# Kernel optimization log

Hardware: AMD Instinct MI355X
Metric: run time of the kernel (lower is better)

## Reference

```python
import jax, jax.numpy as jnp
import numpy as np

N = 2000  # nodes per graph (hardcoded in the original module)


def gatv2(x, src, dst, edge_attr, Wl, Wr, We, att, b):
    """PyG GATv2Conv (concat=True, negative_slope=0.2, edge_dim) forward.
    x: [N, Fin]; src/dst: [E]; edge_attr: [E, 2]; att: [H, C]. Returns [N, H*C]."""
    n = x.shape[0]
    H, C = att.shape
    xl = (x @ Wl).reshape(n, H, C)            # messages from source nodes
    xr = (x @ Wr).reshape(n, H, C)            # target-node term
    ee = (edge_attr @ We).reshape(-1, H, C)   # edge feature term
    m = jax.nn.leaky_relu(xl[src] + xr[dst] + ee, 0.2)
    logits = jnp.einsum('ehc,hc->eh', m, att)           # [E, H]
    lmax = jax.ops.segment_max(logits, dst, num_segments=n)
    p = jnp.exp(logits - lmax[dst])
    denom = jax.ops.segment_sum(p, dst, num_segments=n)
    alpha = p / (denom[dst] + 1e-16)                    # scatter-softmax over in-edges
    out = jax.ops.segment_sum(alpha[:, :, None] * xl[src], dst, num_segments=n)
    return out.reshape(n, H * C) + b


def setup_inputs() -> dict:
    key = jax.random.key(0)
    ks = jax.random.split(key, 32)
    B, T, F, E = 4, 10, 8, 16000
    s = 0.05
    d = {
        'x': jax.random.normal(ks[0], (B, T, N, F), jnp.float32),
        'edge_index': jax.random.randint(ks[1], (2, E), 0, N, jnp.int32),
        'edge_attr': jax.random.normal(ks[2], (E, 2), jnp.float32),
        'w_l0': s * jax.random.normal(ks[3], (8, 128)),
        'w_r0': s * jax.random.normal(ks[4], (8, 128)),
        'w_e0': s * jax.random.normal(ks[5], (2, 128)),
        'att0': s * jax.random.normal(ks[6], (4, 32)),
        'b0': s * jax.random.normal(ks[7], (128,)),
        'w_l1': s * jax.random.normal(ks[8], (128, 128)),
        'w_r1': s * jax.random.normal(ks[9], (128, 128)),
        'w_e1': s * jax.random.normal(ks[10], (2, 128)),
        'att1': s * jax.random.normal(ks[11], (4, 32)),
        'b1': s * jax.random.normal(ks[12], (128,)),
        'w_l2': s * jax.random.normal(ks[13], (128, 32)),
        'w_r2': s * jax.random.normal(ks[14], (128, 32)),
        'w_e2': s * jax.random.normal(ks[15], (2, 32)),
        'att2': s * jax.random.normal(ks[16], (4, 8)),
        'b2': s * jax.random.normal(ks[17], (32,)),
        'w_ih': s * jax.random.normal(ks[18], (1024, 64000)),
        'w_hh': s * jax.random.normal(ks[19], (1024, 256)),
        'b_ih': s * jax.random.normal(ks[20], (1024,)),
        'b_hh': s * jax.random.normal(ks[21], (1024,)),
        'fc1_w': s * jax.random.normal(ks[22], (256, 512)),
        'fc1_b': s * jax.random.normal(ks[23], (512,)),
        'fc2_w': s * jax.random.normal(ks[24], (512, 1)),
        'fc2_b': s * jax.random.normal(ks[25], (1,)),
    }
    return d


def reference(x, edge_index, edge_attr, w_l0, w_r0, w_e0, att0, b0,
              w_l1, w_r1, w_e1, att1, b1, w_l2, w_r2, w_e2, att2, b2,
              w_ih, w_hh, b_ih, b_hh, fc1_w, fc1_b, fc2_w, fc2_b):
    B, T = x.shape[0], x.shape[1]
    # PyG GATv2Conv add_self_loops=True with fill_value='mean' for edge_attr
    loop = jnp.arange(N, dtype=edge_index.dtype)
    src = jnp.concatenate([edge_index[0], loop])
    dst = jnp.concatenate([edge_index[1], loop])
    ea = jnp.concatenate([edge_attr, jnp.broadcast_to(edge_attr.mean(0), (N, 2))], axis=0)

    def gat_stack(xt):  # [N, F] -> [N*32] flattened embedding
        h = jax.nn.relu(gatv2(xt, src, dst, ea, w_l0, w_r0, w_e0, att0, b0))
        h = jax.nn.relu(gatv2(h, src, dst, ea, w_l1, w_r1, w_e1, att1, b1))
        h = jax.nn.relu(gatv2(h, src, dst, ea, w_l2, w_r2, w_e2, att2, b2))
        return h.reshape(-1)

    emb = jax.vmap(jax.vmap(gat_stack))(x)  # [B, T, 64000]

    # single-layer LSTM (torch gate order: i, f, g, o)
    Hh = w_hh.shape[1]
    def step(carry, xt):
        h, c = carry
        g = xt @ w_ih.T + h @ w_hh.T + (b_ih + b_hh)
        i, f, gg, o = jnp.split(g, 4, axis=-1)
        c = jax.nn.sigmoid(f) * c + jax.nn.sigmoid(i) * jnp.tanh(gg)
        h = jax.nn.sigmoid(o) * jnp.tanh(c)
        return (h, c), h
    h0 = jnp.zeros((B, Hh), emb.dtype)
    (_, _), hs = jax.lax.scan(step, (h0, h0), jnp.swapaxes(emb, 0, 1))  # hs: [T, B, Hh]

    last = jax.nn.relu(hs[-1])                       # relu(lstm_out)[:, -1, :]
    hid = jax.nn.relu(last @ fc1_w + fc1_b)          # (dropout=0 -> identity)
    return hid @ fc2_w + fc2_b                       # [B, 1]
```

## Files before the change

### kernel.cpp

```cpp
#include <hip/hip_runtime.h>
#include <hip/hip_bf16.h>
#include <math.h>

typedef __hip_bfloat16 bf16;
typedef __attribute__((ext_vector_type(8))) short short8;
typedef __attribute__((ext_vector_type(4))) float f32x4;

#define NNODES 2000
#define NEDGE_IN 16000
#define NEDGE 18000
#define NGRAPH 40

__device__ __forceinline__ float bf2f(bf16 v){ return __bfloat162float(v); }
__device__ __forceinline__ bf16 f2bf(float v){ return __float2bfloat16(v); }
__device__ __forceinline__ short bfbits(float v){ bf16 t = __float2bfloat16(v); return *reinterpret_cast<short*>(&t); }
__device__ __forceinline__ float blo(unsigned u){ return __uint_as_float(u<<16); }
__device__ __forceinline__ float bhi(unsigned u){ return __uint_as_float(u & 0xffff0000u); }

__global__ __launch_bounds__(256) void k_setup(const float* __restrict__ ea, float* __restrict__ mean_ea,
                        const float* __restrict__ whh, unsigned* __restrict__ whhT2,
                        const float* __restrict__ w1a, const float* __restrict__ w1b,
                        const float* __restrict__ w2a, const float* __restrict__ w2b,
                        bf16* __restrict__ b1a, bf16* __restrict__ b1b,
                        bf16* __restrict__ b2a, bf16* __restrict__ b2b,
                        int* __restrict__ cnt, int* __restrict__ cursor, float* __restrict__ gates){
  int bb = blockIdx.x, tid = threadIdx.x;
  if (bb == 0){
    __shared__ float s0l[256], s1l[256];
    float s0=0.f, s1=0.f;
    for (int e = tid; e < NEDGE_IN; e += 256){ s0 += ea[2*e]; s1 += ea[2*e+1]; }
    s0l[tid]=s0; s1l[tid]=s1; __syncthreads();
    for (int d=128; d>=1; d>>=1){
      if (tid < d){ s0l[tid]+=s0l[tid+d]; s1l[tid]+=s1l[tid+d]; }
      __syncthreads();
    }
    if (tid==0){ mean_ea[0]=s0l[0]/(float)NEDGE_IN; mean_ea[1]=s1l[0]/(float)NEDGE_IN; }
  } else if (bb < 513){
    int idx = (bb-1)*256 + tid;
    int j = idx >> 7, kp = idx & 127;
    unsigned ulo = (unsigned)(unsigned short)bfbits(whh[j*256 + 2*kp]);
    unsigned uhi = (unsigned)(unsigned short)bfbits(whh[j*256 + 2*kp + 1]);
    whhT2[kp*1024 + j] = (uhi<<16) | ulo;
  } else if (bb < 673){
    int idx = (bb-513)*256 + tid;
    const float* src; bf16* dst; int n, local;
    if (idx < 16384){ src=w1a; dst=b1a; n=128; local=idx; }
    else if (idx < 32768){ src=w1b; dst=b1b; n=128; local=idx-16384; }
    else if (idx < 36864){ src=w2a; dst=b2a; n=32; local=idx-32768; }
    else { src=w2b; dst=b2b; n=32; local=idx-36864; }
    int k = local / n, c = local % n;
    dst[c*128 + k] = f2bf(src[local]);
  } else {
    int idx = (bb-673)*256 + tid;
    if (idx < 2000) cnt[idx] = 0;
    else if (idx < 4000) cursor[idx-2000] = 0;
    else if (idx < 44960) gates[idx-4000] = 0.f;
  }
}

__global__ void k_count(const int* __restrict__ ei, int* __restrict__ cnt){
  int e = blockIdx.x*256 + threadIdx.x;
  if (e >= NEDGE) return;
  int d = (e < NEDGE_IN) ? ei[NEDGE_IN + e] : (e - NEDGE_IN);
  atomicAdd(&cnt[d], 1);
}

__global__ void k_scan(const int* __restrict__ cnt, int* __restrict__ off){
  __shared__ int s[2048];
  int lane = threadIdx.x;
  for (int i = lane; i < 2048; i += 64) s[i] = (i < NNODES) ? cnt[i] : 0;
  __syncthreads();
  int base = lane*32, run = 0;
  for (int j=0;j<32;j++){ int t = s[base+j]; s[base+j] = run; run += t; }
  int x = run;
  for (int d=1; d<64; d<<=1){ int y = __shfl_up(x, d); if (lane >= d) x += y; }
  int chunkOff = x - run;
  for (int j=0;j<32;j++){ int idx = base+j; if (idx <= NNODES) off[idx] = chunkOff + s[idx]; }
}

__global__ void k_scatter(const int* __restrict__ ei, const int* __restrict__ off,
                          int* __restrict__ cursor, const float* __restrict__ ea,
                          const float* __restrict__ mean_ea,
                          int* __restrict__ csr_src, float2* __restrict__ eaP){
  int e = blockIdx.x*256 + threadIdx.x;
  if (e >= NEDGE) return;
  int d, sn; float2 a;
  if (e < NEDGE_IN){ sn = ei[e]; d = ei[NEDGE_IN+e]; a = ((const float2*)ea)[e]; }
  else { sn = e-NEDGE_IN; d = sn; a.x = mean_ea[0]; a.y = mean_ea[1]; }
  int p = off[d] + atomicAdd(&cursor[d], 1);
  csr_src[p] = sn;
  eaP[p] = a;
}

__global__ __launch_bounds__(256) void k_gemm0(const float* __restrict__ X, const float* __restrict__ Wa,
                                               const float* __restrict__ Wb,
                                               bf16* __restrict__ Ya, bf16* __restrict__ Yb){
  __shared__ float Ws[2*8*128];
  for (int i = threadIdx.x; i < 8*128; i += 256){ Ws[i] = Wa[i]; Ws[1024+i] = Wb[i]; }
  __syncthreads();
  int j  = threadIdx.x % 128;
  int rg = threadIdx.x / 128;
  size_t m0 = (size_t)blockIdx.x*8 + (size_t)rg*4;
  const float* x0 = X + m0*8;
  float a0=0.f,a1=0.f,a2=0.f,a3=0.f, b0=0.f,b1=0.f,b2=0.f,b3=0.f;
  #pragma unroll
  for (int k=0;k<8;k++){
    float wa = Ws[k*128 + j], wb = Ws[1024 + k*128 + j];
    float x_0 = x0[k], x_1 = x0[8+k], x_2 = x0[16+k], x_3 = x0[24+k];
    a0 += x_0*wa; a1 += x_1*wa; a2 += x_2*wa; a3 += x_3*wa;
    b0 += x_0*wb; b1 += x_1*wb; b2 += x_2*wb; b3 += x_3*wb;
  }
  bf16* ya = Ya + m0*128 + j;
  bf16* yb = Yb + m0*128 + j;
  ya[0]=f2bf(a0); ya[128]=f2bf(a1); ya[256]=f2bf(a2); ya[384]=f2bf(a3);
  yb[0]=f2bf(b0); yb[128]=f2bf(b1); yb[256]=f2bf(b2); yb[384]=f2bf(b3);
}

template<int N>
__global__ __launch_bounds__(256) void k_gemm_mf2(const bf16* __restrict__ A, const bf16* __restrict__ BTa,
                                                  const bf16* __restrict__ BTb,
                                                  bf16* __restrict__ Ya, bf16* __restrict__ Yb){
  const int NT = N/16;
  int lane = threadIdx.x & 63, wv = threadIdx.x >> 6;
  size_t m0 = (size_t)blockIdx.x*128 + (size_t)wv*32;
  int r = lane & 15, kg = lane >> 4;
  const f32x4 zero = {0.f,0.f,0.f,0.f};
  f32x4 acca[2][NT], accb[2][NT];
  #pragma unroll
  for (int s=0;s<2;s++)
    #pragma unroll
    for (int t=0;t<NT;t++){ acca[s][t] = zero; accb[s][t] = zero; }
  #pragma unroll
  for (int c=0;c<4;c++){
    short8 a0 = *(const short8*)(A + (m0 + r)*128 + c*32 + kg*8);
    short8 a1 = *(const short8*)(A + (m0 + 16 + r)*128 + c*32 + kg*8);
    #pragma unroll
    for (int t=0;t<NT;t++){
      short8 ba = *(const short8*)(BTa + (size_t)(t*16 + r)*128 + c*32 + kg*8);
      short8 bb = *(const short8*)(BTb + (size_t)(t*16 + r)*128 + c*32 + kg*8);
      acca[0][t] = __builtin_amdgcn_mfma_f32_16x16x32_bf16(a0, ba, acca[0][t], 0,0,0);
      acca[1][t] = __builtin_amdgcn_mfma_f32_16x16x32_bf16(a1, ba, acca[1][t], 0,0,0);
      accb[0][t] = __builtin_amdgcn_mfma_f32_16x16x32_bf16(a0, bb, accb[0][t], 0,0,0);
      accb[1][t] = __builtin_amdgcn_mfma_f32_16x16x32_bf16(a1, bb, accb[1][t], 0,0,0);
    }
  }
  #pragma unroll
  for (int s=0;s<2;s++)
    #pragma unroll
    for (int t=0;t<NT;t++){
      size_t row = m0 + s*16 + kg*4;
      int col = t*16 + r;
      #pragma unroll
      for (int i=0;i<4;i++){
        Ya[(row+i)*N + col] = f2bf(acca[s][t][i]);
        Yb[(row+i)*N + col] = f2bf(accb[s][t][i]);
      }
    }
}

__global__ __launch_bounds__(256) void k_edge_g(const bf16* __restrict__ XL, const bf16* __restrict__ XR,
                                                const float2* __restrict__ eaP, const int* __restrict__ off,
                                                const int* __restrict__ csr_src, const float* __restrict__ att,
                                                const float* __restrict__ We, const float* __restrict__ bias,
                                                bf16* __restrict__ Hout){
  int tid = threadIdx.x;
  int ln = tid & 63;
  int gq = tid >> 6;
  int n  = blockIdx.x;
  int c0 = 2*ln;
  float av0 = att[c0], av1 = att[c0+1];
  float w00 = We[c0], w01 = We[c0+1];
  float w10 = We[128+c0], w11 = We[128+c0+1];
  const unsigned* XLu = (const unsigned*)XL;
  const unsigned* XRu = (const unsigned*)XR;
  float xr0[10], xr1[10], srun[10], acc0[10], acc1[10];
  #pragma unroll
  for (int t=0;t<10;t++){
    int g = gq*10 + t;
    unsigned xu = XRu[((size_t)g*NNODES + n)*64 + ln];
    xr0[t] = blo(xu); xr1[t] = bhi(xu);
    srun[t]=0.f; acc0[t]=0.f; acc1[t]=0.f;
  }
  int p0 = off[n], p1 = off[n+1];
  for (int p = p0; p < p1; ++p){
    int u = csr_src[p];
    float2 e = eaP[p];
    float ed0 = fmaf(e.x, w00, e.y*w10);
    float ed1 = fmaf(e.x, w01, e.y*w11);
    unsigned xl[10];
    #pragma unroll
    for (int t=0;t<10;t++){
      int g = gq*10 + t;
      xl[t] = XLu[((size_t)g*NNODES + u)*64 + ln];
    }
    #pragma unroll
    for (int t=0;t<10;t++){
      float x0 = blo(xl[t]), x1 = bhi(xl[t]);
      float s0 = x0 + xr0[t] + ed0;
      float s1 = x1 + xr1[t] + ed1;
      float m0 = s0>0.f?s0:0.2f*s0, m1 = s1>0.f?s1:0.2f*s1;
      float c = fmaf(m0, av0, m1*av1);
      #pragma unroll
      for (int d=8; d>=1; d>>=1) c += __shfl_xor(c, d);
      float pe = __expf(c);
      srun[t] += pe;
      acc0[t] = fmaf(pe, x0, acc0[t]);
      acc1[t] = fmaf(pe, x1, acc1[t]);
    }
  }
  #pragma unroll
  for (int t=0;t<10;t++){
    int g = gq*10 + t;
    float inv = 1.f/(srun[t] + 1e-16f);
    float o0 = fmaf(acc0[t], inv, bias[c0]);
    float o1 = fmaf(acc1[t], inv, bias[c0+1]);
    o0 = o0>0.f?o0:0.f; o1 = o1>0.f?o1:0.f;
    unsigned r0 = (unsigned)(unsigned short)bfbits(o0);
    unsigned r1 = (unsigned)(unsigned short)bfbits(o1);
    ((unsigned*)Hout)[((size_t)g*NNODES + n)*64 + ln] = (r1<<16) | r0;
  }
}

template<int H, int C>
__global__ __launch_bounds__(256) void k_edge(const bf16* __restrict__ XL, const bf16* __restrict__ XR,
                                              const float2* __restrict__ eaP, const int* __restrict__ off,
                                              const int* __restrict__ csr_src, const float* __restrict__ att,
                                              const float* __restrict__ We, const float* __restrict__ bias,
                                              bf16* __restrict__ Hout){
  const int HC = H*C;
  const int LPN = HC/2;
  const int NPW = 64/LPN;
  const int NPB = 4*NPW;
  int tid = threadIdx.x;
  int lane = tid & 63, wv = tid >> 6;
  int ln = lane % LPN;
  int n  = blockIdx.x*NPB + wv*NPW + lane/LPN;
  int g  = blockIdx.y;
  int c0 = 2*ln;
  size_t gbase = (size_t)g*NNODES*HC;
  const unsigned* XLu = (const unsigned*)(XL + gbase);
  unsigned xru = ((const unsigned*)(XR + gbase))[n*LPN + ln];
  float xr0 = blo(xru), xr1 = bhi(xru);
  float av0 = att[c0], av1 = att[c0+1];
  float w00 = We[c0], w01 = We[c0+1];
  float w10 = We[HC+c0], w11 = We[HC+c0+1];
  float srun = 0.f, acc0 = 0.f, acc1 = 0.f;
  int p0 = off[n], p1 = off[n+1];
  int p = p0;
  for (; p+2 <= p1; p += 2){
    int uA = csr_src[p], uB = csr_src[p+1];
    float2 eA = eaP[p], eB = eaP[p+1];
    unsigned xlA = XLu[uA*LPN + ln];
    unsigned xlB = XLu[uB*LPN + ln];
    float xa0 = blo(xlA), xa1 = bhi(xlA);
    float xb0 = blo(xlB), xb1 = bhi(xlB);
    float sa0 = xa0 + fmaf(eA.x,w00, fmaf(eA.y,w10, xr0));
    float sa1 = xa1 + fmaf(eA.x,w01, fmaf(eA.y,w11, xr1));
    float sb0 = xb0 + fmaf(eB.x,w00, fmaf(eB.y,w10, xr0));
    float sb1 = xb1 + fmaf(eB.x,w01, fmaf(eB.y,w11, xr1));
    float ma0 = sa0>0.f?sa0:0.2f*sa0, ma1 = sa1>0.f?sa1:0.2f*sa1;
    float mb0 = sb0>0.f?sb0:0.2f*sb0, mb1 = sb1>0.f?sb1:0.2f*sb1;
    float cA = fmaf(ma0,av0, ma1*av1);
    float cB = fmaf(mb0,av0, mb1*av1);
    #pragma unroll
    for (int d=C/4; d>=1; d>>=1){ cA += __shfl_xor(cA, d); cB += __shfl_xor(cB, d); }
    float peA = __expf(cA), peB = __expf(cB);
    srun += peA + peB;
    acc0 = fmaf(peA, xa0, fmaf(peB, xb0, acc0));
    acc1 = fmaf(peA, xa1, fmaf(peB, xb1, acc1));
  }
  if (p < p1){
    int uA = csr_src[p];
    float2 eA = eaP[p];
    unsigned xlA = XLu[uA*LPN + ln];
    float xa0 = blo(xlA), xa1 = bhi(xlA);
    float sa0 = xa0 + fmaf(eA.x,w00, fmaf(eA.y,w10, xr0));
    float sa1 = xa1 + fmaf(eA.x,w01, fmaf(eA.y,w11, xr1));
    float ma0 = sa0>0.f?sa0:0.2f*sa0, ma1 = sa1>0.f?sa1:0.2f*sa1;
    float cA = fmaf(ma0,av0, ma1*av1);
    #pragma unroll
    for (int d=C/4; d>=1; d>>=1) cA += __shfl_xor(cA, d);
    float peA = __expf(cA);
    srun += peA;
    acc0 = fmaf(peA, xa0, acc0);
    acc1 = fmaf(peA, xa1, acc1);
  }
  float inv = 1.f/(srun + 1e-16f);
  float o0 = fmaf(acc0, inv, bias[c0]);
  float o1 = fmaf(acc1, inv, bias[c0+1]);
  o0 = o0>0.f?o0:0.f; o1 = o1>0.f?o1:0.f;
  unsigned r0 = (unsigned)(unsigned short)bfbits(o0);
  unsigned r1 = (unsigned)(unsigned short)bfbits(o1);
  ((unsigned*)(Hout + gbase))[n*LPN + ln] = (r1<<16) | r0;
}

#define GATES_KS 40
__global__ __launch_bounds__(256) void k_gates_mf(const bf16* __restrict__ emb, const float* __restrict__ wih,
                                                  float* __restrict__ gates){
  const int nk = 2000/GATES_KS;
  int lane = threadIdx.x & 63, wv = threadIdx.x >> 6;
  int r = lane & 15, kg = lane >> 4;
  int j0 = (blockIdx.x*4 + wv)*16;
  int k0 = blockIdx.y*nk*32;
  const f32x4 zero = {0.f,0.f,0.f,0.f};
  f32x4 acc0 = zero, acc1 = zero, acc2 = zero;
  const float* wrow = wih + (size_t)(j0 + r)*64000;
  const bf16*  e0p  = emb + (size_t)r*64000;
  const bf16*  e1p  = emb + (size_t)(16+r)*64000;
  const bf16*  e2p  = emb + (size_t)(32+r)*64000;
  #pragma unroll 2
  for (int s=0; s<nk; ++s){
    int k = k0 + s*32 + kg*8;
    float4 wa = *(const float4*)(wrow + k);
    float4 wb = *(const float4*)(wrow + k + 4);
    short8 bfr;
    bfr[0]=bfbits(wa.x); bfr[1]=bfbits(wa.y); bfr[2]=bfbits(wa.z); bfr[3]=bfbits(wa.w);
    bfr[4]=bfbits(wb.x); bfr[5]=bfbits(wb.y); bfr[6]=bfbits(wb.z); bfr[7]=bfbits(wb.w);
    short8 a0 = *(const short8*)(e0p + k);
    short8 a1 = *(const short8*)(e1p + k);
    short8 a2 = *(const short8*)(e2p + k);
    acc0 = __builtin_amdgcn_mfma_f32_16x16x32_bf16(a0, bfr, acc0, 0,0,0);
    acc1 = __builtin_amdgcn_mfma_f32_16x16x32_bf16(a1, bfr, acc1, 0,0,0);
    acc2 = __builtin_amdgcn_mfma_f32_16x16x32_bf16(a2, bfr, acc2, 0,0,0);
  }
  int col = j0 + r;
  #pragma unroll
  for (int i=0;i<4;i++){
    int row = kg*4 + i;
    atomicAdd(&gates[(size_t)row*1024 + col], acc0[i]);
    atomicAdd(&gates[(size_t)(row+16)*1024 + col], acc1[i]);
    if (row + 32 < 40) atomicAdd(&gates[(size_t)(row+32)*1024 + col], acc2[i]);
  }
}

__global__ __launch_bounds__(1024) void k_lstm10(const float* __restrict__ gates, const unsigned* __restrict__ whhT2,
                                                 const float* __restrict__ bih, const float* __restrict__ bhh,
                                                 float* __restrict__ hst){
  __shared__ float hs[256];
  __shared__ float g[1024];
  int b = blockIdx.x, j = threadIdx.x;
  float c_reg = 0.f;
  if (j < 256) hs[j] = 0.f;
  float bias = bih[j] + bhh[j];
  __syncthreads();
  for (int t=0;t<10;t++){
    float acc = gates[(size_t)(b*10+t)*1024 + j] + bias;
    #pragma unroll 16
    for (int kp=0;kp<128;kp++){
      unsigned u = whhT2[kp*1024 + j];
      float2 h2 = *(const float2*)&hs[2*kp];
      acc = fmaf(blo(u), h2.x, acc);
      acc = fmaf(bhi(u), h2.y, acc);
    }
    g[j] = acc;
    __syncthreads();
    if (j < 256){
      float i_ = g[j], f_ = g[j+256], gg = g[j+512], o_ = g[j+768];
      float si = 1.f/(1.f+__expf(-i_));
      float sf = 1.f/(1.f+__expf(-f_));
      float so = 1.f/(1.f+__expf(-o_));
      c_reg = sf*c_reg + si*tanhf(gg);
      float hn = so*tanhf(c_reg);
      hs[j] = hn;
      if (t==9) hst[b*256+j] = hn;
    }
    __syncthreads();
  }
}

__global__ __launch_bounds__(512) void k_head(const float* __restrict__ hst, const float* __restrict__ fc1w,
                                              const float* __restrict__ fc1b, const float* __restrict__ fc2w,
                                              const float* __restrict__ fc2b, float* __restrict__ out){
  __shared__ float r[512];
  int b = blockIdx.x, j = threadIdx.x;
  float acc = fc1b[j];
  for (int k=0;k<256;k++){
    float l = hst[b*256+k]; l = l>0.f?l:0.f;
    acc += l * fc1w[k*512 + j];
  }
  float hid = acc>0.f?acc:0.f;
  r[j] = hid * fc2w[j];
  __syncthreads();
  for (int d=256; d>=1; d>>=1){ if (j<d) r[j]+=r[j+d]; __syncthreads(); }
  if (j==0) out[b] = r[0] + fc2b[0];
}

extern "C" void kernel_launch(void* const* d_in, const int* in_sizes, int n_in,
                              void* d_out, int out_size, void* d_ws, size_t ws_size,
                              hipStream_t stream){
  const float* x    = (const float*)d_in[0];
  const int*   ei   = (const int*)  d_in[1];
  const float* ea   = (const float*)d_in[2];
  const float* wl0  = (const float*)d_in[3];
  const float* wr0  = (const float*)d_in[4];
  const float* we0  = (const float*)d_in[5];
  const float* att0 = (const float*)d_in[6];
  const float* b0   = (const float*)d_in[7];
  const float* wl1  = (const float*)d_in[8];
  const float* wr1  = (const float*)d_in[9];
  const float* we1  = (const float*)d_in[10];
  const float* att1 = (const float*)d_in[11];
  const float* b1   = (const float*)d_in[12];
  const float* wl2  = (const float*)d_in[13];
  const float* wr2  = (const float*)d_in[14];
  const float* we2  = (const float*)d_in[15];
  const float* att2 = (const float*)d_in[16];
  const float* b2   = (const float*)d_in[17];
  const float* wih  = (const float*)d_in[18];
  const float* whh  = (const float*)d_in[19];
  const float* bih  = (const float*)d_in[20];
  const float* bhh  = (const float*)d_in[21];
  const float* fc1w = (const float*)d_in[22];
  const float* fc1b = (const float*)d_in[23];
  const float* fc2w = (const float*)d_in[24];
  const float* fc2b = (const float*)d_in[25];
  float* out = (float*)d_out;

  char* base = (char*)d_ws; size_t cur = 0;
  auto alloc = [&](size_t bytes)->void*{
    cur = (cur + 255) & ~(size_t)255; void* p = base + cur; cur += bytes; return p;
  };
  float* mean_ea = (float*)alloc(8);
  int*   cnt     = (int*)  alloc((size_t)NNODES*4);
  int*   off     = (int*)  alloc((size_t)(NNODES+1)*4);
  int*   cursor  = (int*)  alloc((size_t)NNODES*4);
  int*   csr_src = (int*)  alloc((size_t)NEDGE*4);
  float2* eaP    = (float2*)alloc((size_t)NEDGE*8);
  bf16*  XL      = (bf16*) alloc((size_t)80000*128*2);
  bf16*  XR      = (bf16*) alloc((size_t)80000*128*2);
  bf16*  HBUF    = (bf16*) alloc((size_t)80000*128*2);
  float* gates   = (float*)alloc((size_t)40*1024*4);
  float* hst     = (float*)alloc(4*256*4);
  unsigned* whhT2= (unsigned*)alloc((size_t)128*1024*4);
  bf16*  bt1a    = (bf16*) alloc((size_t)128*128*2);
  bf16*  bt1b    = (bf16*) alloc((size_t)128*128*2);
  bf16*  bt2a    = (bf16*) alloc((size_t)32*128*2);
  bf16*  bt2b    = (bf16*) alloc((size_t)32*128*2);

  k_setup <<<849,256,0,stream>>>(ea, mean_ea, whh, whhT2, wl1, wr1, wl2, wr2,
                                 bt1a, bt1b, bt2a, bt2b, cnt, cursor, gates);
  k_count   <<<(NEDGE+255)/256,256,0,stream>>>(ei, cnt);
  k_scan    <<<1,64,0,stream>>>(cnt, off);
  k_scatter <<<(NEDGE+255)/256,256,0,stream>>>(ei, off, cursor, ea, mean_ea, csr_src, eaP);

  k_gemm0   <<<10000,256,0,stream>>>(x, wl0, wr0, XL, XR);
  k_edge_g  <<<NNODES,256,0,stream>>>(XL,XR,eaP,off,csr_src,att0,we0,b0,HBUF);

  k_gemm_mf2<128> <<<625,256,0,stream>>>(HBUF, bt1a, bt1b, XL, XR);
  k_edge_g  <<<NNODES,256,0,stream>>>(XL,XR,eaP,off,csr_src,att1,we1,b1,HBUF);

  k_gemm_mf2<32> <<<625,256,0,stream>>>(HBUF, bt2a, bt2b, XL, XR);
  k_edge<4,8> <<<dim3(125,40),256,0,stream>>>(XL,XR,eaP,off,csr_src,att2,we2,b2,HBUF);

  k_gates_mf<<<dim3(16,GATES_KS),256,0,stream>>>(HBUF, wih, gates);

  k_lstm10<<<4,1024,0,stream>>>(gates, whhT2, bih, bhh, hst);

  k_head<<<4,512,0,stream>>>(hst, fc1w, fc1b, fc2w, fc2b, out);
}
```

Baseline: 417.7 us.

## Fuse gemm0 into setup, split-K gates with partial buffer, fuse LSTM with head

The layer-0 projection GEMM is merged into the setup kernel as extra blocks, which removes one launch. The gates split-K count doubles and atomicAdd accumulation is replaced by per-split partial writes plus a separate reduction kernel, which also drops the gates zeroing. The LSTM and the FC head are merged into one kernel. Leaky-relu and relu selects become fmaxf. The cost is an extra reduction pass over a larger partial buffer, in exchange for more parallelism in the gates GEMM and no atomic contention.

```diff
diff --git a/kernel.cpp b/kernel.cpp
--- a/kernel.cpp
+++ b/kernel.cpp
@@ -10,6 +10,7 @@
 #define NEDGE_IN 16000
 #define NEDGE 18000
 #define NGRAPH 40
+#define GATES_KS 80
 
 __device__ __forceinline__ float bf2f(bf16 v){ return __bfloat162float(v); }
 __device__ __forceinline__ bf16 f2bf(float v){ return __float2bfloat16(v); }
@@ -23,10 +24,34 @@
                         const float* __restrict__ w2a, const float* __restrict__ w2b,
                         bf16* __restrict__ b1a, bf16* __restrict__ b1b,
                         bf16* __restrict__ b2a, bf16* __restrict__ b2b,
-                        int* __restrict__ cnt, int* __restrict__ cursor, float* __restrict__ gates){
+                        int* __restrict__ cnt, int* __restrict__ cursor,
+                        const float* __restrict__ X, const float* __restrict__ Wa,
+                        const float* __restrict__ Wb,
+                        bf16* __restrict__ Ya, bf16* __restrict__ Yb){
+  __shared__ float smem[2048];
   int bb = blockIdx.x, tid = threadIdx.x;
-  if (bb == 0){
-    __shared__ float s0l[256], s1l[256];
+  if (bb >= 689){
+    int blk = bb - 689;
+    for (int i = tid; i < 1024; i += 256){ smem[i] = Wa[i]; smem[1024+i] = Wb[i]; }
+    __syncthreads();
+    int j  = tid & 127;
+    int rg = tid >> 7;
+    size_t m0 = (size_t)blk*8 + (size_t)rg*4;
+    const float* x0 = X + m0*8;
+    float a0=0.f,a1=0.f,a2=0.f,a3=0.f, b0=0.f,b1=0.f,b2=0.f,b3=0.f;
+    #pragma unroll
+    for (int k=0;k<8;k++){
+      float wa = smem[k*128 + j], wb = smem[1024 + k*128 + j];
+      float x_0 = x0[k], x_1 = x0[8+k], x_2 = x0[16+k], x_3 = x0[24+k];
+      a0 += x_0*wa; a1 += x_1*wa; a2 += x_2*wa; a3 += x_3*wa;
+      b0 += x_0*wb; b1 += x_1*wb; b2 += x_2*wb; b3 += x_3*wb;
+    }
+    bf16* ya = Ya + m0*128 + j;
+    bf16* yb = Yb + m0*128 + j;
+    ya[0]=f2bf(a0); ya[128]=f2bf(a1); ya[256]=f2bf(a2); ya[384]=f2bf(a3);
+    yb[0]=f2bf(b0); yb[128]=f2bf(b1); yb[256]=f2bf(b2); yb[384]=f2bf(b3);
+  } else if (bb == 0){
+    float* s0l = smem; float* s1l = smem + 256;
     float s0=0.f, s1=0.f;
     for (int e = tid; e < NEDGE_IN; e += 256){ s0 += ea[2*e]; s1 += ea[2*e+1]; }
     s0l[tid]=s0; s1l[tid]=s1; __syncthreads();
@@ -54,7 +79,6 @@
     int idx = (bb-673)*256 + tid;
     if (idx < 2000) cnt[idx] = 0;
     else if (idx < 4000) cursor[idx-2000] = 0;
-    else if (idx < 44960) gates[idx-4000] = 0.f;
   }
 }
 
@@ -90,30 +114,6 @@
   int p = off[d] + atomicAdd(&cursor[d], 1);
   csr_src[p] = sn;
   eaP[p] = a;
-}
-
-__global__ __launch_bounds__(256) void k_gemm0(const float* __restrict__ X, const float* __restrict__ Wa,
-                                               const float* __restrict__ Wb,
-                                               bf16* __restrict__ Ya, bf16* __restrict__ Yb){
-  __shared__ float Ws[2*8*128];
-  for (int i = threadIdx.x; i < 8*128; i += 256){ Ws[i] = Wa[i]; Ws[1024+i] = Wb[i]; }
-  __syncthreads();
-  int j  = threadIdx.x % 128;
-  int rg = threadIdx.x / 128;
-  size_t m0 = (size_t)blockIdx.x*8 + (size_t)rg*4;
-  const float* x0 = X + m0*8;
-  float a0=0.f,a1=0.f,a2=0.f,a3=0.f, b0=0.f,b1=0.f,b2=0.f,b3=0.f;
-  #pragma unroll
-  for (int k=0;k<8;k++){
-    float wa = Ws[k*128 + j], wb = Ws[1024 + k*128 + j];
-    float x_0 = x0[k], x_1 = x0[8+k], x_2 = x0[16+k], x_3 = x0[24+k];
-    a0 += x_0*wa; a1 += x_1*wa; a2 += x_2*wa; a3 += x_3*wa;
-    b0 += x_0*wb; b1 += x_1*wb; b2 += x_2*wb; b3 += x_3*wb;
-  }
-  bf16* ya = Ya + m0*128 + j;
-  bf16* yb = Yb + m0*128 + j;
-  ya[0]=f2bf(a0); ya[128]=f2bf(a1); ya[256]=f2bf(a2); ya[384]=f2bf(a3);
-  yb[0]=f2bf(b0); yb[128]=f2bf(b1); yb[256]=f2bf(b2); yb[384]=f2bf(b3);
 }
 
 template<int N>
@@ -198,7 +198,8 @@
       float x0 = blo(xl[t]), x1 = bhi(xl[t]);
       float s0 = x0 + xr0[t] + ed0;
       float s1 = x1 + xr1[t] + ed1;
-      float m0 = s0>0.f?s0:0.2f*s0, m1 = s1>0.f?s1:0.2f*s1;
+      float m0 = fmaxf(s0, 0.2f*s0);
+      float m1 = fmaxf(s1, 0.2f*s1);
       float c = fmaf(m0, av0, m1*av1);
       #pragma unroll
       for (int d=8; d>=1; d>>=1) c += __shfl_xor(c, d);
@@ -214,7 +215,7 @@
     float inv = 1.f/(srun[t] + 1e-16f);
     float o0 = fmaf(acc0[t], inv, bias[c0]);
     float o1 = fmaf(acc1[t], inv, bias[c0+1]);
-    o0 = o0>0.f?o0:0.f; o1 = o1>0.f?o1:0.f;
+    o0 = fmaxf(o0, 0.f); o1 = fmaxf(o1, 0.f);
     unsigned r0 = (unsigned)(unsigned short)bfbits(o0);
     unsigned r1 = (unsigned)(unsigned short)bfbits(o1);
     ((unsigned*)Hout)[((size_t)g*NNODES + n)*64 + ln] = (r1<<16) | r0;
@@ -258,8 +259,8 @@
     float sa1 = xa1 + fmaf(eA.x,w01, fmaf(eA.y,w11, xr1));
     float sb0 = xb0 + fmaf(eB.x,w00, fmaf(eB.y,w10, xr0));
     float sb1 = xb1 + fmaf(eB.x,w01, fmaf(eB.y,w11, xr1));
-    float ma0 = sa0>0.f?sa0:0.2f*sa0, ma1 = sa1>0.f?sa1:0.2f*sa1;
-    float mb0 = sb0>0.f?sb0:0.2f*sb0, mb1 = sb1>0.f?sb1:0.2f*sb1;
+    float ma0 = fmaxf(sa0, 0.2f*sa0), ma1 = fmaxf(sa1, 0.2f*sa1);
+    float mb0 = fmaxf(sb0, 0.2f*sb0), mb1 = fmaxf(sb1, 0.2f*sb1);
     float cA = fmaf(ma0,av0, ma1*av1);
     float cB = fmaf(mb0,av0, mb1*av1);
     #pragma unroll
@@ -276,7 +277,7 @@
     float xa0 = blo(xlA), xa1 = bhi(xlA);
     float sa0 = xa0 + fmaf(eA.x,w00, fmaf(eA.y,w10, xr0));
     float sa1 = xa1 + fmaf(eA.x,w01, fmaf(eA.y,w11, xr1));
-    float ma0 = sa0>0.f?sa0:0.2f*sa0, ma1 = sa1>0.f?sa1:0.2f*sa1;
+    float ma0 = fmaxf(sa0, 0.2f*sa0), ma1 = fmaxf(sa1, 0.2f*sa1);
     float cA = fmaf(ma0,av0, ma1*av1);
     #pragma unroll
     for (int d=C/4; d>=1; d>>=1) cA += __shfl_xor(cA, d);
@@ -288,20 +289,20 @@
   float inv = 1.f/(srun + 1e-16f);
   float o0 = fmaf(acc0, inv, bias[c0]);
   float o1 = fmaf(acc1, inv, bias[c0+1]);
-  o0 = o0>0.f?o0:0.f; o1 = o1>0.f?o1:0.f;
+  o0 = fmaxf(o0, 0.f); o1 = fmaxf(o1, 0.f);
   unsigned r0 = (unsigned)(unsigned short)bfbits(o0);
   unsigned r1 = (unsigned)(unsigned short)bfbits(o1);
   ((unsigned*)(Hout + gbase))[n*LPN + ln] = (r1<<16) | r0;
 }
 
-#define GATES_KS 40
 __global__ __launch_bounds__(256) void k_gates_mf(const bf16* __restrict__ emb, const float* __restrict__ wih,
-                                                  float* __restrict__ gates){
+                                                  float* __restrict__ part){
   const int nk = 2000/GATES_KS;
   int lane = threadIdx.x & 63, wv = threadIdx.x >> 6;
   int r = lane & 15, kg = lane >> 4;
   int j0 = (blockIdx.x*4 + wv)*16;
-  int k0 = blockIdx.y*nk*32;
+  int ks = blockIdx.y;
+  int k0 = ks*nk*32;
   const f32x4 zero = {0.f,0.f,0.f,0.f};
   f32x4 acc0 = zero, acc1 = zero, acc2 = zero;
   const float* wrow = wih + (size_t)(j0 + r)*64000;
@@ -324,18 +325,29 @@
     acc2 = __builtin_amdgcn_mfma_f32_16x16x32_bf16(a2, bfr, acc2, 0,0,0);
   }
   int col = j0 + r;
+  float* prow = part + (size_t)ks*40960;
   #pragma unroll
   for (int i=0;i<4;i++){
     int row = kg*4 + i;
-    atomicAdd(&gates[(size_t)row*1024 + col], acc0[i]);
-    atomicAdd(&gates[(size_t)(row+16)*1024 + col], acc1[i]);
-    if (row + 32 < 40) atomicAdd(&gates[(size_t)(row+32)*1024 + col], acc2[i]);
-  }
-}
-
-__global__ __launch_bounds__(1024) void k_lstm10(const float* __restrict__ gates, const unsigned* __restrict__ whhT2,
-                                                 const float* __restrict__ bih, const float* __restrict__ bhh,
-                                                 float* __restrict__ hst){
+    prow[(size_t)row*1024 + col] = acc0[i];
+    prow[(size_t)(row+16)*1024 + col] = acc1[i];
+    if (row + 32 < 40) prow[(size_t)(row+32)*1024 + col] = acc2[i];
+  }
+}
+
+__global__ __launch_bounds__(256) void k_gred(const float* __restrict__ part, float* __restrict__ gates){
+  int idx = blockIdx.x*256 + threadIdx.x;
+  float s = 0.f;
+  #pragma unroll 8
+  for (int ks=0; ks<GATES_KS; ks++) s += part[(size_t)ks*40960 + idx];
+  gates[idx] = s;
+}
+
+__global__ __launch_bounds__(1024) void k_lstm10h(const float* __restrict__ gates, const unsigned* __restrict__ whhT2,
+                                                  const float* __restrict__ bih, const float* __restrict__ bhh,
+                                                  const float* __restrict__ fc1w, const float* __restrict__ fc1b,
+                                                  const float* __restrict__ fc2w, const float* __restrict__ fc2b,
+                                                  float* __restrict__ out){
   __shared__ float hs[256];
   __shared__ float g[1024];
   int b = blockIdx.x, j = threadIdx.x;
@@ -360,29 +372,25 @@
       float sf = 1.f/(1.f+__expf(-f_));
       float so = 1.f/(1.f+__expf(-o_));
       c_reg = sf*c_reg + si*tanhf(gg);
-      float hn = so*tanhf(c_reg);
-      hs[j] = hn;
-      if (t==9) hst[b*256+j] = hn;
+      hs[j] = so*tanhf(c_reg);
     }
     __syncthreads();
   }
-}
-
-__global__ __launch_bounds__(512) void k_head(const float* __restrict__ hst, const float* __restrict__ fc1w,
-                                              const float* __restrict__ fc1b, const float* __restrict__ fc2w,
-                                              const float* __restrict__ fc2b, float* __restrict__ out){
-  __shared__ float r[512];
-  int b = blockIdx.x, j = threadIdx.x;
-  float acc = fc1b[j];
-  for (int k=0;k<256;k++){
-    float l = hst[b*256+k]; l = l>0.f?l:0.f;
-    acc += l * fc1w[k*512 + j];
-  }
-  float hid = acc>0.f?acc:0.f;
-  r[j] = hid * fc2w[j];
+  if (j < 512){
+    float acc = fc1b[j];
+    for (int k=0;k<256;k++){
+      float l = fmaxf(hs[k], 0.f);
+      acc = fmaf(l, fc1w[k*512 + j], acc);
+    }
+    float hid = fmaxf(acc, 0.f);
+    g[j] = hid * fc2w[j];
+  }
   __syncthreads();
-  for (int d=256; d>=1; d>>=1){ if (j<d) r[j]+=r[j+d]; __syncthreads(); }
-  if (j==0) out[b] = r[0] + fc2b[0];
+  for (int d=256; d>=1; d>>=1){
+    if (j < d) g[j] += g[j+d];
+    __syncthreads();
+  }
+  if (j==0) out[b] = g[0] + fc2b[0];
 }
 
 extern "C" void kernel_launch(void* const* d_in, const int* in_sizes, int n_in,
@@ -429,21 +437,21 @@
   bf16*  XL      = (bf16*) alloc((size_t)80000*128*2);
   bf16*  XR      = (bf16*) alloc((size_t)80000*128*2);
   bf16*  HBUF    = (bf16*) alloc((size_t)80000*128*2);
+  float* part    = (float*)alloc((size_t)GATES_KS*40960*4);
   float* gates   = (float*)alloc((size_t)40*1024*4);
-  float* hst     = (float*)alloc(4*256*4);
   unsigned* whhT2= (unsigned*)alloc((size_t)128*1024*4);
   bf16*  bt1a    = (bf16*) alloc((size_t)128*128*2);
   bf16*  bt1b    = (bf16*) alloc((size_t)128*128*2);
   bf16*  bt2a    = (bf16*) alloc((size_t)32*128*2);
   bf16*  bt2b    = (bf16*) alloc((size_t)32*128*2);
 
-  k_setup <<<849,256,0,stream>>>(ea, mean_ea, whh, whhT2, wl1, wr1, wl2, wr2,
-                                 bt1a, bt1b, bt2a, bt2b, cnt, cursor, gates);
+  k_setup <<<10689,256,0,stream>>>(ea, mean_ea, whh, whhT2, wl1, wr1, wl2, wr2,
+                                   bt1a, bt1b, bt2a, bt2b, cnt, cursor,
+                                   x, wl0, wr0, XL, XR);
   k_count   <<<(NEDGE+255)/256,256,0,stream>>>(ei, cnt);
   k_scan    <<<1,64,0,stream>>>(cnt, off);
   k_scatter <<<(NEDGE+255)/256,256,0,stream>>>(ei, off, cursor, ea, mean_ea, csr_src, eaP);
 
-  k_gemm0   <<<10000,256,0,stream>>>(x, wl0, wr0, XL, XR);
   k_edge_g  <<<NNODES,256,0,stream>>>(XL,XR,eaP,off,csr_src,att0,we0,b0,HBUF);
 
   k_gemm_mf2<128> <<<625,256,0,stream>>>(HBUF, bt1a, bt1b, XL, XR);
@@ -452,9 +460,8 @@
   k_gemm_mf2<32> <<<625,256,0,stream>>>(HBUF, bt2a, bt2b, XL, XR);
   k_edge<4,8> <<<dim3(125,40),256,0,stream>>>(XL,XR,eaP,off,csr_src,att2,we2,b2,HBUF);
 
-  k_gates_mf<<<dim3(16,GATES_KS),256,0,stream>>>(HBUF, wih, gates);
-
-  k_lstm10<<<4,1024,0,stream>>>(gates, whhT2, bih, bhh, hst);
-
-  k_head<<<4,512,0,stream>>>(hst, fc1w, fc1b, fc2w, fc2b, out);
-}
+  k_gates_mf<<<dim3(16,GATES_KS),256,0,stream>>>(HBUF, wih, part);
+  k_gred    <<<160,256,0,stream>>>(part, gates);
+
+  k_lstm10h<<<4,1024,0,stream>>>(gates, whhT2, bih, bhh, fc1w, fc1b, fc2w, fc2b, out);
+}
```

New measurement: 419.1 us. About the same (+0.3%).
